# Kernel optimization log

Measured on AMD Instinct MI355X. Metric: run time of the kernel, lower is better.

The kernel has to match this reference:

```python
import jax, jax.numpy as jnp
import numpy as np

B, N = 8, 64
EMB, CD, NL = 32, 24, 3          # emb_dim, cloud_dim, output degrees l=0,1,2 (cloudord)
NB, H = 3, 100                   # radial basis count, radial hidden width
RADIUS = 2.0                     # neighborradius
CLOUD_OUT = CD * NL**2 + EMB     # 24*9 + 32 = 248 (cloud_res concat)
RES_OUT = 2 * CLOUD_OUT          # 496 (AtomResiduals doubles channels)
FF = 128                         # ffl1size // 1


def spherical_harmonics(u):
    # real SH on unit vectors, se3cnn component order (y,z,x for l=1)
    x, y, z = u[..., 0], u[..., 1], u[..., 2]
    Y0 = jnp.full(x.shape + (1,), 0.28209479177, dtype=u.dtype)
    c1 = 0.48860251190
    Y1 = c1 * jnp.stack([y, z, x], -1)
    c2a, c2b = 1.09254843059, 0.31539156525
    Y2 = jnp.stack([c2a * x * y, c2a * y * z, c2b * (3.0 * z * z - 1.0),
                    c2a * x * z, 0.5 * c2a * (x * x - y * y)], -1)
    return [Y0, Y1, Y2]


def setup_inputs() -> dict:
    key = jax.random.key(0)
    ks = jax.random.split(key, 12)
    g = lambda i, shape, s=0.1: jax.random.normal(ks[i], shape, jnp.float32) * s
    return dict(
        xyz=jax.random.normal(ks[0], (B, N, 3), jnp.float32),
        features=jax.random.randint(ks[1], (B, N), 0, 6),
        emb=g(2, (6, EMB), 1.0),
        rW1=g(3, (NB, H)), rb1=jnp.zeros((H,), jnp.float32),
        rW2=g(4, (H, H)), rb2=jnp.zeros((H,), jnp.float32),
        rW3=g(5, (H, NL * CD * EMB)), rb3=jnp.zeros((NL * CD * EMB,), jnp.float32),
        resW=g(6, (CLOUD_OUT, CLOUD_OUT)), resb=jnp.zeros((CLOUD_OUT,), jnp.float32),
        res_gamma=jnp.ones((CLOUD_OUT,), jnp.float32),
        res_beta=jnp.zeros((CLOUD_OUT,), jnp.float32),
        cW=g(7, (RES_OUT, FF)), cb=jnp.zeros((FF,), jnp.float32),
        c_gamma=jnp.ones((FF,), jnp.float32), c_beta=jnp.zeros((FF,), jnp.float32),
        oW=g(8, (FF, 1)), ob=jnp.zeros((1,), jnp.float32),
    )


def reference(xyz, features, emb, rW1, rb1, rW2, rb2, rW3, rb3,
              resW, resb, res_gamma, res_beta, cW, cb, c_gamma, c_beta, oW, ob):
    eps = 1e-8
    f = emb[features]                                     # [B,N,EMB] scalar (l=0) features
    rij = xyz[:, None, :, :] - xyz[:, :, None, :]         # r_j - r_i  [B,N,N,3]
    d = jnp.sqrt(jnp.sum(rij * rij, -1) + eps)            # [B,N,N]
    mask = ((d < RADIUS) & (~jnp.eye(N, dtype=bool))).astype(f.dtype)
    # CosineBasisModel: cos^2 bumps centered at linspace(0, RADIUS, NB)
    radii = jnp.linspace(0.0, RADIUS, NB)
    step = radii[1] - radii[0]
    u = jnp.abs(d[..., None] - radii) / step
    basis = jnp.where(u < 1.0, jnp.cos(0.5 * jnp.pi * u) ** 2, 0.0)  # [B,N,N,NB]
    sp = lambda x: jax.nn.softplus(5.0 * x) / 5.0          # rescaled Softplus(beta=5)
    h = sp(basis @ rW1 + rb1)
    h = sp(h @ rW2 + rb2)
    R = (h @ rW3 + rb3).reshape(B, N, N, NL, CD, EMB)      # per-pair radial weights
    # contract scalar input channels first (keeps intermediates small): [B,N,N,L,U]
    t = jnp.einsum('bijluv,bjv->bijlu', R, f) / jnp.sqrt(float(EMB))
    Ys = spherical_harmonics(rij / d[..., None])
    inv = (1.0 / jnp.sqrt(jnp.maximum(mask.sum(-1), 1.0)))[:, :, None, None]
    outs = []
    for l, Y in enumerate(Ys):
        o = jnp.einsum('bij,bijm,biju->bium', mask, Y, t[..., l, :])  # [B,N,U,2l+1]
        outs.append((o * inv).reshape(B, N, CD * (2 * l + 1)))
    conv = jnp.concatenate(outs, -1)                       # [B,N,216]
    feats = jnp.concatenate([f, conv], -1)                 # cloud_res concat [B,N,248]
    # AtomResiduals: Linear -> BatchNorm(batch stats) -> relu, concat with input
    x2 = feats.reshape(B * N, CLOUD_OUT) @ resW + resb
    mu, var = x2.mean(0), x2.var(0)
    x2 = jax.nn.relu((x2 - mu) / jnp.sqrt(var + 1e-5) * res_gamma + res_beta)
    feats = jnp.concatenate([feats, x2.reshape(B, N, CLOUD_OUT)], -1)  # [B,N,496]
    pooled = feats.mean(1)                                 # mean collation [B,496]
    h2 = jax.nn.leaky_relu(pooled @ cW + cb, 0.01)
    mu2, var2 = h2.mean(0), h2.var(0)
    h2 = jax.nn.leaky_relu((h2 - mu2) / jnp.sqrt(var2 + 1e-5) * c_gamma + c_beta, 0.01)
    return jax.nn.sigmoid(h2 @ oW + ob)                    # [B,1]
```

## Files before the change

kernel.cpp:

```cpp
#include <hip/hip_runtime.h>
#include <hip/hip_bf16.h>

#define BB   8
#define NN   64
#define EMB  32
#define CD   24
#define HH   100
#define LU   72
#define COUT 248
#define RESO 496
#define FF   128

__device__ __forceinline__ float sp5(float x) {
    float z = 5.0f * x;
    float t = __expf(-fabsf(z));
    return 0.2f * (fmaxf(z, 0.0f) + __logf(1.0f + t));
}
__device__ __forceinline__ float4 ld4(const float* p) { return *reinterpret_cast<const float4*>(p); }
__device__ __forceinline__ void st4(float* p, float4 v) { *reinterpret_cast<float4*>(p) = v; }
__device__ __forceinline__ void fma4(float4& a, float s, float4 w) {
    a.x = fmaf(s, w.x, a.x); a.y = fmaf(s, w.y, a.y);
    a.z = fmaf(s, w.z, a.z); a.w = fmaf(s, w.w, a.w);
}

__global__ __launch_bounds__(256) void k0_w3f(
    const float* __restrict__ rW3, const float* __restrict__ rb3,
    const float* __restrict__ emb, float* __restrict__ W3f_all, float* __restrict__ tb_all,
    float* __restrict__ accz)
{
    if (blockIdx.x == 0) {
        for (int idx = threadIdx.x; idx < 2 * COUT + BB * COUT + RESO * BB; idx += 256)
            accz[idx] = 0.f;
    }
    const int t = blockIdx.x / 10, kc = blockIdx.x % 10;
    __shared__ float embt[EMB];
    if (threadIdx.x < EMB) embt[threadIdx.x] = emb[t * EMB + threadIdx.x];
    __syncthreads();
    for (int idx = threadIdx.x; idx < 10 * LU; idx += 256) {
        const int k = kc * 10 + idx / LU, lu = idx % LU;
        const float* w = rW3 + (size_t)k * (LU * EMB) + lu * EMB;
        float acc = 0.f;
#pragma unroll
        for (int v4 = 0; v4 < EMB / 4; ++v4) {
            float4 wv = ld4(w + 4 * v4);
            acc += wv.x * embt[4 * v4] + wv.y * embt[4 * v4 + 1]
                 + wv.z * embt[4 * v4 + 2] + wv.w * embt[4 * v4 + 3];
        }
        W3f_all[(size_t)t * HH * LU + k * LU + lu] = acc;
    }
    if (kc == 0 && threadIdx.x < LU) {
        const float* w = rb3 + threadIdx.x * EMB;
        float acc = 0.f;
        for (int v = 0; v < EMB; ++v) acc += w[v] * embt[v];
        tb_all[t * LU + threadIdx.x] = acc;
    }
}

__global__ __launch_bounds__(256) void k1_pairs(
    const float* __restrict__ xyz, const int* __restrict__ feat,
    const float* __restrict__ rW1, const float* __restrict__ rb1,
    const float* __restrict__ rW2, const float* __restrict__ rb2,
    const float* __restrict__ W3f_all, const float* __restrict__ tb_all,
    float* __restrict__ tbufJ)
{
    const int b = blockIdx.x >> 6, j = blockIdx.x & 63;
    const int tid = threadIdx.x;

    __shared__ __align__(16) float W3fs[HH * LU];
    __shared__ __align__(16) float h1T[HH * NN];
    __shared__ __align__(16) float h2T[HH * NN];
    __shared__ __align__(16) float xi[NN * 3];

    const int type = feat[b * NN + j];
    {
        const float* src = W3f_all + (size_t)type * HH * LU;
        for (int idx = tid; idx < HH * LU / 4; idx += 256) st4(&W3fs[idx * 4], ld4(&src[idx * 4]));
    }
    if (tid < 48) st4(&xi[tid * 4], ld4(&xyz[b * NN * 3 + tid * 4]));
    __syncthreads();

    {
        const int ik = tid & 63, ug = tid >> 6;
        const float dx = xi[j * 3 + 0] - xi[ik * 3 + 0];
        const float dy = xi[j * 3 + 1] - xi[ik * 3 + 1];
        const float dz = xi[j * 3 + 2] - xi[ik * 3 + 2];
        const float d = sqrtf(dx * dx + dy * dy + dz * dz + 1e-8f);
        float bas[3];
#pragma unroll
        for (int r = 0; r < 3; ++r) {
            float u = fabsf(d - (float)r);
            float c = cosf(1.57079632679489662f * u);
            bas[r] = (u < 1.0f) ? c * c : 0.0f;
        }
#pragma unroll 5
        for (int uu = 0; uu < 25; ++uu) {
            const int u = ug * 25 + uu;
            float v = rb1[u] + bas[0] * rW1[u] + bas[1] * rW1[HH + u] + bas[2] * rW1[2 * HH + u];
            h1T[u * NN + ik] = sp5(v);
        }
    }
    __syncthreads();

    if (tid < 200) {
        const int ut = tid % 25, ig = tid / 25;
        float4 a[8];
        {
            float4 b0 = ld4(&rb2[4 * ut]);
#pragma unroll
            for (int m = 0; m < 8; ++m) a[m] = b0;
        }
#pragma unroll 4
        for (int k = 0; k < HH; ++k) {
            float4 w  = ld4(&rW2[k * HH + 4 * ut]);
            float4 hA = ld4(&h1T[k * NN + 8 * ig]);
            float4 hB = ld4(&h1T[k * NN + 8 * ig + 4]);
            fma4(a[0], hA.x, w); fma4(a[1], hA.y, w); fma4(a[2], hA.z, w); fma4(a[3], hA.w, w);
            fma4(a[4], hB.x, w); fma4(a[5], hB.y, w); fma4(a[6], hB.z, w); fma4(a[7], hB.w, w);
        }
#pragma unroll
        for (int m = 0; m < 8; ++m) {
            a[m].x = sp5(a[m].x); a[m].y = sp5(a[m].y); a[m].z = sp5(a[m].z); a[m].w = sp5(a[m].w);
        }
        st4(&h2T[(4 * ut + 0) * NN + 8 * ig],     make_float4(a[0].x, a[1].x, a[2].x, a[3].x));
        st4(&h2T[(4 * ut + 0) * NN + 8 * ig + 4], make_float4(a[4].x, a[5].x, a[6].x, a[7].x));
        st4(&h2T[(4 * ut + 1) * NN + 8 * ig],     make_float4(a[0].y, a[1].y, a[2].y, a[3].y));
        st4(&h2T[(4 * ut + 1) * NN + 8 * ig + 4], make_float4(a[4].y, a[5].y, a[6].y, a[7].y));
        st4(&h2T[(4 * ut + 2) * NN + 8 * ig],     make_float4(a[0].z, a[1].z, a[2].z, a[3].z));
        st4(&h2T[(4 * ut + 2) * NN + 8 * ig + 4], make_float4(a[4].z, a[5].z, a[6].z, a[7].z));
        st4(&h2T[(4 * ut + 3) * NN + 8 * ig],     make_float4(a[0].w, a[1].w, a[2].w, a[3].w));
        st4(&h2T[(4 * ut + 3) * NN + 8 * ig + 4], make_float4(a[4].w, a[5].w, a[6].w, a[7].w));
    }
    __syncthreads();

    if (tid < 144) {
        const int lut = tid % 18, ig = tid / 18;
        float4 a[8];
        {
            float4 t0 = ld4(&tb_all[type * LU + 4 * lut]);
#pragma unroll
            for (int m = 0; m < 8; ++m) a[m] = t0;
        }
#pragma unroll 4
        for (int k = 0; k < HH; ++k) {
            float4 w  = ld4(&W3fs[k * LU + 4 * lut]);
            float4 hA = ld4(&h2T[k * NN + 8 * ig]);
            float4 hB = ld4(&h2T[k * NN + 8 * ig + 4]);
            fma4(a[0], hA.x, w); fma4(a[1], hA.y, w); fma4(a[2], hA.z, w); fma4(a[3], hA.w, w);
            fma4(a[4], hB.x, w); fma4(a[5], hB.y, w); fma4(a[6], hB.z, w); fma4(a[7], hB.w, w);
        }
        const float s = 0.17677669529663688f;
        float* base = &tbufJ[((size_t)(b * NN + j)) * (NN * LU)];
#pragma unroll
        for (int m = 0; m < 8; ++m) {
            const int i = 8 * ig + m;
            st4(&base[i * LU + 4 * lut], make_float4(a[m].x * s, a[m].y * s, a[m].z * s, a[m].w * s));
        }
    }
}

__global__ __launch_bounds__(256) void k2_conv(
    const float* __restrict__ xyz, const int* __restrict__ feat,
    const float* __restrict__ emb, const float* __restrict__ tbufJ,
    const float* __restrict__ resW, const float* __restrict__ resb,
    float* __restrict__ x2pre, float* __restrict__ colsum,
    float* __restrict__ colsq, float* __restrict__ pooledF)
{
    const int b = blockIdx.x >> 6, i = blockIdx.x & 63;
    const int tid = threadIdx.x;
    __shared__ __align__(16) float xj[NN * 3];
    __shared__ __align__(16) float mYT[9 * 68];
    __shared__ __align__(16) float tlT[LU * 68];
    __shared__ __align__(16) float fs[COUT];
    __shared__ float inv_s;

    if (tid < 48) st4(&xj[tid * 4], ld4(&xyz[b * NN * 3 + tid * 4]));
    if (tid >= 64 && tid < 96) fs[tid - 64] = emb[feat[b * NN + i] * EMB + (tid - 64)];
    {
        for (int idx = tid; idx < NN * LU; idx += 256) {
            const int jj = idx / LU, lu = idx - jj * LU;
            tlT[lu * 68 + jj] = tbufJ[((size_t)(b * NN + jj)) * (NN * LU) + i * LU + lu];
        }
    }
    __syncthreads();
    if (tid < 64) {
        const int jj = tid;
        float dx = xj[jj * 3 + 0] - xj[i * 3 + 0];
        float dy = xj[jj * 3 + 1] - xj[i * 3 + 1];
        float dz = xj[jj * 3 + 2] - xj[i * 3 + 2];
        float d = sqrtf(dx * dx + dy * dy + dz * dz + 1e-8f);
        float m = (d < 2.0f && jj != i) ? 1.0f : 0.0f;
        float ux = dx / d, uy = dy / d, uz = dz / d;
        mYT[0 * 68 + jj] = m * 0.28209479177f;
        mYT[1 * 68 + jj] = m * 0.48860251190f * uy;
        mYT[2 * 68 + jj] = m * 0.48860251190f * uz;
        mYT[3 * 68 + jj] = m * 0.48860251190f * ux;
        mYT[4 * 68 + jj] = m * 1.09254843059f * ux * uy;
        mYT[5 * 68 + jj] = m * 1.09254843059f * uy * uz;
        mYT[6 * 68 + jj] = m * 0.31539156525f * (3.0f * uz * uz - 1.0f);
        mYT[7 * 68 + jj] = m * 1.09254843059f * ux * uz;
        mYT[8 * 68 + jj] = m * 0.54627421529f * (ux * ux - uy * uy);
        unsigned long long bal = __ballot(m > 0.5f);
        if (jj == 0) inv_s = rsqrtf(fmaxf((float)__popcll(bal), 1.0f));
    }
    __syncthreads();

    if (tid < 216) {
        int l, u, m, yoff;
        if (tid < 24)      { l = 0; u = tid; m = 0; yoff = 0; }
        else if (tid < 96) { int q = tid - 24; l = 1; u = q / 3; m = q % 3; yoff = 1; }
        else               { int q = tid - 96; l = 2; u = q / 5; m = q % 5; yoff = 4; }
        const int lu = l * CD + u, yr = yoff + m;
        float acc = 0.f;
#pragma unroll
        for (int j4 = 0; j4 < 16; ++j4) {
            float4 y = ld4(&mYT[yr * 68 + 4 * j4]);
            float4 t = ld4(&tlT[lu * 68 + 4 * j4]);
            acc += y.x * t.x + y.y * t.y + y.z * t.z + y.w * t.w;
        }
        fs[EMB + tid] = acc * inv_s;
    }
    __syncthreads();

    if (tid < COUT) {
        float acc = resb[tid];
        for (int k = 0; k < COUT; ++k) acc = fmaf(fs[k], resW[k * COUT + tid], acc);
        x2pre[(size_t)blockIdx.x * COUT + tid] = acc;
        atomicAdd(&colsum[tid], acc);
        atomicAdd(&colsq[tid], acc * acc);
        atomicAdd(&pooledF[b * COUT + tid], fs[tid]);
    }
}

__global__ __launch_bounds__(256) void k5_pool(
    const float* __restrict__ x2pre, const float* __restrict__ colsum,
    const float* __restrict__ colsq, const float* __restrict__ pooledF,
    const float* __restrict__ gamma, const float* __restrict__ beta,
    float* __restrict__ pooledT)
{
    const int b = blockIdx.x >> 3, seg = blockIdx.x & 7;
    const int c = threadIdx.x;
    if (c >= COUT) return;
    if (seg == 0) pooledT[c * BB + b] = pooledF[b * COUT + c] * (1.0f / (float)NN);
    const float mu   = colsum[c] * (1.0f / 512.0f);
    const float var  = colsq[c] * (1.0f / 512.0f) - mu * mu;
    const float rstd = 1.0f / sqrtf(var + 1e-5f);
    const float g = gamma[c], be = beta[c];
    float acc = 0.f;
#pragma unroll
    for (int ii = 0; ii < 8; ++ii) {
        const int i = seg * 8 + ii;
        const float v = (x2pre[(size_t)(b * NN + i) * COUT + c] - mu) * rstd * g + be;
        acc += fmaxf(v, 0.f);
    }
    atomicAdd(&pooledT[(COUT + c) * BB + b], acc * (1.0f / (float)NN));
}

__global__ __launch_bounds__(1024) void k6_head(
    const float* __restrict__ pooledT,
    const float* __restrict__ cW, const float* __restrict__ cb,
    const float* __restrict__ c_gamma, const float* __restrict__ c_beta,
    const float* __restrict__ oW, const float* __restrict__ ob,
    float* __restrict__ out)
{
    const int tid = threadIdx.x;
    const int o = tid & 127, chunk = tid >> 7;
    __shared__ __align__(16) float psT[RESO * BB];
    __shared__ __align__(16) float part[8 * 8 * FF];
    __shared__ __align__(16) float red[FF * BB];
    for (int idx = tid; idx < RESO * BB / 4; idx += 1024) st4(&psT[idx * 4], ld4(&pooledT[idx * 4]));
    __syncthreads();

    float4 aA = make_float4(0.f, 0.f, 0.f, 0.f), aB = aA;
    const int kbase = chunk * 62;
#pragma unroll 2
    for (int kk = 0; kk < 62; ++kk) {
        const int k = kbase + kk;
        const float w = cW[k * FF + o];
        fma4(aA, w, ld4(&psT[k * BB]));
        fma4(aB, w, ld4(&psT[k * BB + 4]));
    }
    part[0 * 1024 + chunk * FF + o] = aA.x;
    part[1 * 1024 + chunk * FF + o] = aA.y;
    part[2 * 1024 + chunk * FF + o] = aA.z;
    part[3 * 1024 + chunk * FF + o] = aA.w;
    part[4 * 1024 + chunk * FF + o] = aB.x;
    part[5 * 1024 + chunk * FF + o] = aB.y;
    part[6 * 1024 + chunk * FF + o] = aB.z;
    part[7 * 1024 + chunk * FF + o] = aB.w;
    __syncthreads();

    if (tid < FF) {
        float h[8];
#pragma unroll
        for (int q = 0; q < 8; ++q) {
            float s = 0.f;
#pragma unroll
            for (int ch = 0; ch < 8; ++ch) s += part[q * 1024 + ch * FF + tid];
            h[q] = s + cb[tid];
        }
        float mu = 0.f;
#pragma unroll
        for (int q = 0; q < 8; ++q) { h[q] = (h[q] >= 0.f) ? h[q] : 0.01f * h[q]; mu += h[q]; }
        mu *= 0.125f;
        float var = 0.f;
#pragma unroll
        for (int q = 0; q < 8; ++q) { float dd = h[q] - mu; var += dd * dd; }
        var *= 0.125f;
        const float rstd = 1.0f / sqrtf(var + 1e-5f);
        const float g = c_gamma[tid], be = c_beta[tid], wo = oW[tid];
#pragma unroll
        for (int q = 0; q < 8; ++q) {
            float v = (h[q] - mu) * rstd * g + be;
            h[q] = ((v >= 0.f) ? v : 0.01f * v) * wo;
        }
        st4(&red[tid * 8],     make_float4(h[0], h[1], h[2], h[3]));
        st4(&red[tid * 8 + 4], make_float4(h[4], h[5], h[6], h[7]));
    }
    __syncthreads();
    for (int off = 64; off >= 1; off >>= 1) {
        if (tid < off) {
            float4 x0 = ld4(&red[tid * 8]),     y0 = ld4(&red[(tid + off) * 8]);
            float4 x1 = ld4(&red[tid * 8 + 4]), y1 = ld4(&red[(tid + off) * 8 + 4]);
            st4(&red[tid * 8],     make_float4(x0.x + y0.x, x0.y + y0.y, x0.z + y0.z, x0.w + y0.w));
            st4(&red[tid * 8 + 4], make_float4(x1.x + y1.x, x1.y + y1.y, x1.z + y1.z, x1.w + y1.w));
        }
        __syncthreads();
    }
    if (tid < BB) out[tid] = 1.0f / (1.0f + __expf(-(red[tid] + ob[0])));
}

extern "C" void kernel_launch(void* const* d_in, const int* in_sizes, int n_in,
                              void* d_out, int out_size, void* d_ws, size_t ws_size,
                              hipStream_t stream)
{
    const float* xyz  = (const float*)d_in[0];
    const int*   feat = (const int*)  d_in[1];
    const float* emb  = (const float*)d_in[2];
    const float* rW1  = (const float*)d_in[3];
    const float* rb1  = (const float*)d_in[4];
    const float* rW2  = (const float*)d_in[5];
    const float* rb2  = (const float*)d_in[6];
    const float* rW3  = (const float*)d_in[7];
    const float* rb3  = (const float*)d_in[8];
    const float* resW = (const float*)d_in[9];
    const float* resb = (const float*)d_in[10];
    const float* res_gamma = (const float*)d_in[11];
    const float* res_beta  = (const float*)d_in[12];
    const float* cW   = (const float*)d_in[13];
    const float* cb   = (const float*)d_in[14];
    const float* c_gamma = (const float*)d_in[15];
    const float* c_beta  = (const float*)d_in[16];
    const float* oW   = (const float*)d_in[17];
    const float* ob   = (const float*)d_in[18];
    float* out = (float*)d_out;

    char* ws = (char*)d_ws;
    float* tbufJ   = (float*)ws;
    float* W3f_all = (float*)(ws + 9437184);
    float* tb_all  = (float*)(ws + 9437184 + 172800);
    float* x2pre   = (float*)(ws + 9437184 + 172800 + 1728);
    float* colsum  = x2pre + 512 * COUT;
    float* colsq   = colsum + COUT;
    float* pooledF = colsq + COUT;
    float* pooledT = pooledF + BB * COUT;

    k0_w3f  <<<60, 256, 0, stream>>>(rW3, rb3, emb, W3f_all, tb_all, colsum);
    k1_pairs<<<BB * NN, 256, 0, stream>>>(xyz, feat, rW1, rb1, rW2, rb2, W3f_all, tb_all, tbufJ);
    k2_conv <<<BB * NN, 256, 0, stream>>>(xyz, feat, emb, tbufJ, resW, resb,
                                          x2pre, colsum, colsq, pooledF);
    k5_pool <<<BB * 8, 256, 0, stream>>>(x2pre, colsum, colsq, pooledF,
                                         res_gamma, res_beta, pooledT);
    k6_head <<<1, 1024, 0, stream>>>(pooledT, cW, cb, c_gamma, c_beta, oW, ob, out);
}
```

Baseline: 175.5 us.

## Replace per-pair radial MLP with per-type distance lookup table and interpolation

Instead of evaluating the radial MLP for every atom pair, the radial network output is precomputed for each atom type on a grid of 2048 distances in [0,3]. The conv kernel then linearly interpolates from that table. This removes most of the per-pair matmul work and the large pairwise intermediate buffer, at the cost of interpolation error. The atomics for BatchNorm statistics and pooling are also replaced by a dedicated stats kernel and per-segment partial sums, which adds one extra launch.

```diff
diff --git a/kernel.cpp b/kernel.cpp
--- a/kernel.cpp
+++ b/kernel.cpp
@@ -10,6 +10,7 @@
 #define COUT 248
 #define RESO 496
 #define FF   128
+#define TT   2048
 
 __device__ __forceinline__ float sp5(float x) {
     float z = 5.0f * x;
@@ -23,15 +24,10 @@
     a.z = fmaf(s, w.z, a.z); a.w = fmaf(s, w.w, a.w);
 }
 
-__global__ __launch_bounds__(256) void k0_w3f(
+__global__ __launch_bounds__(256) void k0a_w3f(
     const float* __restrict__ rW3, const float* __restrict__ rb3,
-    const float* __restrict__ emb, float* __restrict__ W3f_all, float* __restrict__ tb_all,
-    float* __restrict__ accz)
-{
-    if (blockIdx.x == 0) {
-        for (int idx = threadIdx.x; idx < 2 * COUT + BB * COUT + RESO * BB; idx += 256)
-            accz[idx] = 0.f;
-    }
+    const float* __restrict__ emb, float* __restrict__ W3f_all, float* __restrict__ tb_all)
+{
     const int t = blockIdx.x / 10, kc = blockIdx.x % 10;
     __shared__ float embt[EMB];
     if (threadIdx.x < EMB) embt[threadIdx.x] = emb[t * EMB + threadIdx.x];
@@ -56,35 +52,29 @@
     }
 }
 
-__global__ __launch_bounds__(256) void k1_pairs(
-    const float* __restrict__ xyz, const int* __restrict__ feat,
+__global__ __launch_bounds__(256) void k0b_lut(
     const float* __restrict__ rW1, const float* __restrict__ rb1,
     const float* __restrict__ rW2, const float* __restrict__ rb2,
     const float* __restrict__ W3f_all, const float* __restrict__ tb_all,
-    float* __restrict__ tbufJ)
-{
-    const int b = blockIdx.x >> 6, j = blockIdx.x & 63;
+    float* __restrict__ LUT)
+{
+    const int bt = blockIdx.x >> 5, chunk = blockIdx.x & 31;
+    const int s0 = chunk * 64;
     const int tid = threadIdx.x;
 
     __shared__ __align__(16) float W3fs[HH * LU];
-    __shared__ __align__(16) float h1T[HH * NN];
-    __shared__ __align__(16) float h2T[HH * NN];
-    __shared__ __align__(16) float xi[NN * 3];
-
-    const int type = feat[b * NN + j];
+    __shared__ __align__(16) float h1T[HH * 64];
+    __shared__ __align__(16) float h2T[HH * 64];
+
     {
-        const float* src = W3f_all + (size_t)type * HH * LU;
+        const float* src = W3f_all + (size_t)bt * HH * LU;
         for (int idx = tid; idx < HH * LU / 4; idx += 256) st4(&W3fs[idx * 4], ld4(&src[idx * 4]));
     }
-    if (tid < 48) st4(&xi[tid * 4], ld4(&xyz[b * NN * 3 + tid * 4]));
     __syncthreads();
 
     {
         const int ik = tid & 63, ug = tid >> 6;
-        const float dx = xi[j * 3 + 0] - xi[ik * 3 + 0];
-        const float dy = xi[j * 3 + 1] - xi[ik * 3 + 1];
-        const float dz = xi[j * 3 + 2] - xi[ik * 3 + 2];
-        const float d = sqrtf(dx * dx + dy * dy + dz * dz + 1e-8f);
+        const float d = (float)(s0 + ik) * (3.0f / 2047.0f);
         float bas[3];
 #pragma unroll
         for (int r = 0; r < 3; ++r) {
@@ -96,7 +86,7 @@
         for (int uu = 0; uu < 25; ++uu) {
             const int u = ug * 25 + uu;
             float v = rb1[u] + bas[0] * rW1[u] + bas[1] * rW1[HH + u] + bas[2] * rW1[2 * HH + u];
-            h1T[u * NN + ik] = sp5(v);
+            h1T[u * 64 + ik] = sp5(v);
         }
     }
     __syncthreads();
@@ -112,8 +102,8 @@
 #pragma unroll 4
         for (int k = 0; k < HH; ++k) {
             float4 w  = ld4(&rW2[k * HH + 4 * ut]);
-            float4 hA = ld4(&h1T[k * NN + 8 * ig]);
-            float4 hB = ld4(&h1T[k * NN + 8 * ig + 4]);
+            float4 hA = ld4(&h1T[k * 64 + 8 * ig]);
+            float4 hB = ld4(&h1T[k * 64 + 8 * ig + 4]);
             fma4(a[0], hA.x, w); fma4(a[1], hA.y, w); fma4(a[2], hA.z, w); fma4(a[3], hA.w, w);
             fma4(a[4], hB.x, w); fma4(a[5], hB.y, w); fma4(a[6], hB.z, w); fma4(a[7], hB.w, w);
         }
@@ -121,14 +111,14 @@
         for (int m = 0; m < 8; ++m) {
             a[m].x = sp5(a[m].x); a[m].y = sp5(a[m].y); a[m].z = sp5(a[m].z); a[m].w = sp5(a[m].w);
         }
-        st4(&h2T[(4 * ut + 0) * NN + 8 * ig],     make_float4(a[0].x, a[1].x, a[2].x, a[3].x));
-        st4(&h2T[(4 * ut + 0) * NN + 8 * ig + 4], make_float4(a[4].x, a[5].x, a[6].x, a[7].x));
-        st4(&h2T[(4 * ut + 1) * NN + 8 * ig],     make_float4(a[0].y, a[1].y, a[2].y, a[3].y));
-        st4(&h2T[(4 * ut + 1) * NN + 8 * ig + 4], make_float4(a[4].y, a[5].y, a[6].y, a[7].y));
-        st4(&h2T[(4 * ut + 2) * NN + 8 * ig],     make_float4(a[0].z, a[1].z, a[2].z, a[3].z));
-        st4(&h2T[(4 * ut + 2) * NN + 8 * ig + 4], make_float4(a[4].z, a[5].z, a[6].z, a[7].z));
-        st4(&h2T[(4 * ut + 3) * NN + 8 * ig],     make_float4(a[0].w, a[1].w, a[2].w, a[3].w));
-        st4(&h2T[(4 * ut + 3) * NN + 8 * ig + 4], make_float4(a[4].w, a[5].w, a[6].w, a[7].w));
+        st4(&h2T[(4 * ut + 0) * 64 + 8 * ig],     make_float4(a[0].x, a[1].x, a[2].x, a[3].x));
+        st4(&h2T[(4 * ut + 0) * 64 + 8 * ig + 4], make_float4(a[4].x, a[5].x, a[6].x, a[7].x));
+        st4(&h2T[(4 * ut + 1) * 64 + 8 * ig],     make_float4(a[0].y, a[1].y, a[2].y, a[3].y));
+        st4(&h2T[(4 * ut + 1) * 64 + 8 * ig + 4], make_float4(a[4].y, a[5].y, a[6].y, a[7].y));
+        st4(&h2T[(4 * ut + 2) * 64 + 8 * ig],     make_float4(a[0].z, a[1].z, a[2].z, a[3].z));
+        st4(&h2T[(4 * ut + 2) * 64 + 8 * ig + 4], make_float4(a[4].z, a[5].z, a[6].z, a[7].z));
+        st4(&h2T[(4 * ut + 3) * 64 + 8 * ig],     make_float4(a[0].w, a[1].w, a[2].w, a[3].w));
+        st4(&h2T[(4 * ut + 3) * 64 + 8 * ig + 4], make_float4(a[4].w, a[5].w, a[6].w, a[7].w));
     }
     __syncthreads();
 
@@ -136,52 +126,49 @@
         const int lut = tid % 18, ig = tid / 18;
         float4 a[8];
         {
-            float4 t0 = ld4(&tb_all[type * LU + 4 * lut]);
+            float4 t0 = ld4(&tb_all[bt * LU + 4 * lut]);
 #pragma unroll
             for (int m = 0; m < 8; ++m) a[m] = t0;
         }
 #pragma unroll 4
         for (int k = 0; k < HH; ++k) {
             float4 w  = ld4(&W3fs[k * LU + 4 * lut]);
-            float4 hA = ld4(&h2T[k * NN + 8 * ig]);
-            float4 hB = ld4(&h2T[k * NN + 8 * ig + 4]);
+            float4 hA = ld4(&h2T[k * 64 + 8 * ig]);
+            float4 hB = ld4(&h2T[k * 64 + 8 * ig + 4]);
             fma4(a[0], hA.x, w); fma4(a[1], hA.y, w); fma4(a[2], hA.z, w); fma4(a[3], hA.w, w);
             fma4(a[4], hB.x, w); fma4(a[5], hB.y, w); fma4(a[6], hB.z, w); fma4(a[7], hB.w, w);
         }
         const float s = 0.17677669529663688f;
-        float* base = &tbufJ[((size_t)(b * NN + j)) * (NN * LU)];
+        float* base = LUT + ((size_t)bt * TT + s0) * LU;
 #pragma unroll
         for (int m = 0; m < 8; ++m) {
-            const int i = 8 * ig + m;
-            st4(&base[i * LU + 4 * lut], make_float4(a[m].x * s, a[m].y * s, a[m].z * s, a[m].w * s));
+            const int smp = 8 * ig + m;
+            st4(&base[smp * LU + 4 * lut], make_float4(a[m].x * s, a[m].y * s, a[m].z * s, a[m].w * s));
         }
     }
 }
 
 __global__ __launch_bounds__(256) void k2_conv(
     const float* __restrict__ xyz, const int* __restrict__ feat,
-    const float* __restrict__ emb, const float* __restrict__ tbufJ,
+    const float* __restrict__ emb, const float* __restrict__ LUT,
     const float* __restrict__ resW, const float* __restrict__ resb,
-    float* __restrict__ x2pre, float* __restrict__ colsum,
-    float* __restrict__ colsq, float* __restrict__ pooledF)
+    float* __restrict__ feats, float* __restrict__ x2pre)
 {
     const int b = blockIdx.x >> 6, i = blockIdx.x & 63;
     const int tid = threadIdx.x;
     __shared__ __align__(16) float xj[NN * 3];
+    __shared__ int   tys[NN];
+    __shared__ float dpos[NN];
     __shared__ __align__(16) float mYT[9 * 68];
     __shared__ __align__(16) float tlT[LU * 68];
     __shared__ __align__(16) float fs[COUT];
     __shared__ float inv_s;
 
     if (tid < 48) st4(&xj[tid * 4], ld4(&xyz[b * NN * 3 + tid * 4]));
-    if (tid >= 64 && tid < 96) fs[tid - 64] = emb[feat[b * NN + i] * EMB + (tid - 64)];
-    {
-        for (int idx = tid; idx < NN * LU; idx += 256) {
-            const int jj = idx / LU, lu = idx - jj * LU;
-            tlT[lu * 68 + jj] = tbufJ[((size_t)(b * NN + jj)) * (NN * LU) + i * LU + lu];
-        }
-    }
-    __syncthreads();
+    if (tid >= 64 && tid < 128) tys[tid - 64] = feat[b * NN + (tid - 64)];
+    if (tid >= 128 && tid < 160) fs[tid - 128] = emb[feat[b * NN + i] * EMB + (tid - 128)];
+    __syncthreads();
+
     if (tid < 64) {
         const int jj = tid;
         float dx = xj[jj * 3 + 0] - xj[i * 3 + 0];
@@ -199,8 +186,20 @@
         mYT[6 * 68 + jj] = m * 0.31539156525f * (3.0f * uz * uz - 1.0f);
         mYT[7 * 68 + jj] = m * 1.09254843059f * ux * uz;
         mYT[8 * 68 + jj] = m * 0.54627421529f * (ux * ux - uy * uy);
+        dpos[jj] = fminf(d, 3.0f) * (2047.0f / 3.0f);
         unsigned long long bal = __ballot(m > 0.5f);
         if (jj == 0) inv_s = rsqrtf(fmaxf((float)__popcll(bal), 1.0f));
+    }
+    __syncthreads();
+
+    for (int idx = tid; idx < NN * LU; idx += 256) {
+        const int jj = idx / LU, lu = idx - jj * LU;
+        const float pos = dpos[jj];
+        int i0 = (int)pos; i0 = (i0 > TT - 2) ? (TT - 2) : i0;
+        const float fr = pos - (float)i0;
+        const float* rowp = LUT + ((size_t)tys[jj] * TT + i0) * LU + lu;
+        const float v0 = rowp[0], v1 = rowp[LU];
+        tlT[lu * 68 + jj] = v0 + fr * (v1 - v0);
     }
     __syncthreads();
 
@@ -222,41 +221,77 @@
     __syncthreads();
 
     if (tid < COUT) {
+        const size_t row = (size_t)blockIdx.x;
+        feats[row * COUT + tid] = fs[tid];
         float acc = resb[tid];
-        for (int k = 0; k < COUT; ++k) acc = fmaf(fs[k], resW[k * COUT + tid], acc);
-        x2pre[(size_t)blockIdx.x * COUT + tid] = acc;
-        atomicAdd(&colsum[tid], acc);
-        atomicAdd(&colsq[tid], acc * acc);
-        atomicAdd(&pooledF[b * COUT + tid], fs[tid]);
-    }
-}
-
-__global__ __launch_bounds__(256) void k5_pool(
-    const float* __restrict__ x2pre, const float* __restrict__ colsum,
-    const float* __restrict__ colsq, const float* __restrict__ pooledF,
+#pragma unroll 4
+        for (int k4 = 0; k4 < COUT / 4; ++k4) {
+            float4 f4 = ld4(&fs[4 * k4]);
+            acc = fmaf(f4.x, resW[(4 * k4 + 0) * COUT + tid], acc);
+            acc = fmaf(f4.y, resW[(4 * k4 + 1) * COUT + tid], acc);
+            acc = fmaf(f4.z, resW[(4 * k4 + 2) * COUT + tid], acc);
+            acc = fmaf(f4.w, resW[(4 * k4 + 3) * COUT + tid], acc);
+        }
+        x2pre[row * COUT + tid] = acc;
+    }
+}
+
+__global__ __launch_bounds__(256) void k4_stats(
+    const float* __restrict__ x2pre, float* __restrict__ stats)
+{
+    const int c0 = blockIdx.x * 8;
+    const int col = threadIdx.x & 7, r0 = threadIdx.x >> 3;
+    float s = 0.f, s2 = 0.f;
+#pragma unroll
+    for (int p = 0; p < 16; ++p) {
+        const int r = r0 + 32 * p;
+        const float v = x2pre[(size_t)r * COUT + c0 + col];
+        s += v; s2 += v * v;
+    }
+    __shared__ float rs[256], rq[256];
+    rs[threadIdx.x] = s; rq[threadIdx.x] = s2;
+    __syncthreads();
+    for (int off = 128; off >= 8; off >>= 1) {
+        if (threadIdx.x < off) { rs[threadIdx.x] += rs[threadIdx.x + off]; rq[threadIdx.x] += rq[threadIdx.x + off]; }
+        __syncthreads();
+    }
+    if (threadIdx.x < 8) {
+        const float mu  = rs[threadIdx.x] * (1.0f / 512.0f);
+        const float var = rq[threadIdx.x] * (1.0f / 512.0f) - mu * mu;
+        stats[c0 + threadIdx.x]        = mu;
+        stats[COUT + c0 + threadIdx.x] = 1.0f / sqrtf(var + 1e-5f);
+    }
+}
+
+__global__ __launch_bounds__(512) void k5_pool(
+    const float* __restrict__ feats, const float* __restrict__ x2pre,
+    const float* __restrict__ stats,
     const float* __restrict__ gamma, const float* __restrict__ beta,
-    float* __restrict__ pooledT)
+    float* __restrict__ pp)
 {
     const int b = blockIdx.x >> 3, seg = blockIdx.x & 7;
     const int c = threadIdx.x;
-    if (c >= COUT) return;
-    if (seg == 0) pooledT[c * BB + b] = pooledF[b * COUT + c] * (1.0f / (float)NN);
-    const float mu   = colsum[c] * (1.0f / 512.0f);
-    const float var  = colsq[c] * (1.0f / 512.0f) - mu * mu;
-    const float rstd = 1.0f / sqrtf(var + 1e-5f);
-    const float g = gamma[c], be = beta[c];
+    if (c >= RESO) return;
     float acc = 0.f;
-#pragma unroll
-    for (int ii = 0; ii < 8; ++ii) {
-        const int i = seg * 8 + ii;
-        const float v = (x2pre[(size_t)(b * NN + i) * COUT + c] - mu) * rstd * g + be;
-        acc += fmaxf(v, 0.f);
-    }
-    atomicAdd(&pooledT[(COUT + c) * BB + b], acc * (1.0f / (float)NN));
+    if (c < COUT) {
+#pragma unroll
+        for (int ii = 0; ii < 8; ++ii)
+            acc += feats[(size_t)(b * NN + seg * 8 + ii) * COUT + c];
+    } else {
+        const int cc = c - COUT;
+        const float mu = stats[cc], rstd = stats[COUT + cc];
+        const float g = gamma[cc], be = beta[cc];
+#pragma unroll
+        for (int ii = 0; ii < 8; ++ii) {
+            const float v = (x2pre[(size_t)(b * NN + seg * 8 + ii) * COUT + cc] - mu) * rstd * g + be;
+            acc += fmaxf(v, 0.f);
+        }
+    }
+    pp[(seg * BB + b) * RESO + c] = acc * (1.0f / (float)NN);
 }
 
 __global__ __launch_bounds__(1024) void k6_head(
-    const float* __restrict__ pooledT,
+    const float* __restrict__ pp,
     const float* __restrict__ cW, const float* __restrict__ cb,
     const float* __restrict__ c_gamma, const float* __restrict__ c_beta,
     const float* __restrict__ oW, const float* __restrict__ ob,
@@ -267,7 +302,13 @@
     __shared__ __align__(16) float psT[RESO * BB];
     __shared__ __align__(16) float part[8 * 8 * FF];
     __shared__ __align__(16) float red[FF * BB];
-    for (int idx = tid; idx < RESO * BB / 4; idx += 1024) st4(&psT[idx * 4], ld4(&pooledT[idx * 4]));
+    for (int idx = tid; idx < RESO * BB; idx += 1024) {
+        const int bb = idx / RESO, k = idx - bb * RESO;
+        float s = 0.f;
+#pragma unroll
+        for (int seg = 0; seg < 8; ++seg) s += pp[seg * (BB * RESO) + idx];
+        psT[k * BB + bb] = s;
+    }
     __syncthreads();
 
     float4 aA = make_float4(0.f, 0.f, 0.f, 0.f), aB = aA;
@@ -355,20 +396,18 @@
     float* out = (float*)d_out;
 
     char* ws = (char*)d_ws;
-    float* tbufJ   = (float*)ws;
-    float* W3f_all = (float*)(ws + 9437184);
-    float* tb_all  = (float*)(ws + 9437184 + 172800);
-    float* x2pre   = (float*)(ws + 9437184 + 172800 + 1728);
-    float* colsum  = x2pre + 512 * COUT;
-    float* colsq   = colsum + COUT;
-    float* pooledF = colsq + COUT;
-    float* pooledT = pooledF + BB * COUT;
-
-    k0_w3f  <<<60, 256, 0, stream>>>(rW3, rb3, emb, W3f_all, tb_all, colsum);
-    k1_pairs<<<BB * NN, 256, 0, stream>>>(xyz, feat, rW1, rb1, rW2, rb2, W3f_all, tb_all, tbufJ);
-    k2_conv <<<BB * NN, 256, 0, stream>>>(xyz, feat, emb, tbufJ, resW, resb,
-                                          x2pre, colsum, colsq, pooledF);
-    k5_pool <<<BB * 8, 256, 0, stream>>>(x2pre, colsum, colsq, pooledF,
-                                         res_gamma, res_beta, pooledT);
-    k6_head <<<1, 1024, 0, stream>>>(pooledT, cW, cb, c_gamma, c_beta, oW, ob, out);
-}
+    float* LUT     = (float*)ws;
+    float* W3f_all = (float*)(ws + 3538944);
+    float* tb_all  = (float*)(ws + 3711744);
+    float* feats   = (float*)(ws + 3713472);
+    float* x2pre   = (float*)(ws + 4221376);
+    float* stats   = (float*)(ws + 4729280);
+    float* pp      = (float*)(ws + 4731264);
+
+    k0a_w3f <<<60, 256, 0, stream>>>(rW3, rb3, emb, W3f_all, tb_all);
+    k0b_lut <<<192, 256, 0, stream>>>(rW1, rb1, rW2, rb2, W3f_all, tb_all, LUT);
+    k2_conv <<<BB * NN, 256, 0, stream>>>(xyz, feat, emb, LUT, resW, resb, feats, x2pre);
+    k4_stats<<<31, 256, 0, stream>>>(x2pre, stats);
+    k5_pool <<<BB * 8, 512, 0, stream>>>(feats, x2pre, stats, res_gamma, res_beta, pp);
+    k6_head <<<1, 1024, 0, stream>>>(pp, cW, cb, c_gamma, c_beta, oW, ob, out);
+}
```

After: 157.8 us. 10.1% less time.
